# Kernel tuning notes

Hardware: AMD Instinct MI355X
Metric: run time of the kernel (lower is better)

## Reference

```python
import jax, jax.numpy as jnp
import numpy as np

N = 100000   # nodes
E = 1600000  # edges (before self loops)
H = 4        # heads
C = 32       # per-head channels
D = H * C    # hidden_dim = 128
G = 64       # graphs in batch
L = 4        # num_layers
IN_DIM = 7
NEG_SLOPE = 0.2


def setup_inputs() -> dict:
    key = jax.random.key(0)
    ks = jax.random.split(key, 14)
    s = 0.1
    x = jax.random.normal(ks[0], (N, IN_DIM), jnp.float32)
    edge_index = jax.random.randint(ks[1], (2, E), 0, N, dtype=jnp.int32)
    batch = jnp.sort(jax.random.randint(ks[2], (N,), 0, G, dtype=jnp.int32))
    W0 = jax.random.normal(ks[3], (IN_DIM, D), jnp.float32) * s
    a_src0 = jax.random.normal(ks[4], (H, C), jnp.float32) * s
    a_dst0 = jax.random.normal(ks[5], (H, C), jnp.float32) * s
    b0 = jnp.zeros((D,), jnp.float32)
    Ws = jax.random.normal(ks[6], (L - 1, D, D), jnp.float32) * s
    a_srcs = jax.random.normal(ks[7], (L - 1, H, C), jnp.float32) * s
    a_dsts = jax.random.normal(ks[8], (L - 1, H, C), jnp.float32) * s
    bs = jnp.zeros((L - 1, D), jnp.float32)
    ln_g = jnp.ones((L, D), jnp.float32)
    ln_b = jnp.zeros((L, D), jnp.float32)
    return dict(x=x, edge_index=edge_index, batch=batch, W0=W0, a_src0=a_src0,
                a_dst0=a_dst0, b0=b0, Ws=Ws, a_srcs=a_srcs, a_dsts=a_dsts,
                bs=bs, ln_g=ln_g, ln_b=ln_b)


def _gat_layer(x, W, a_src, a_dst, b, src, dst):
    # x: [N, F_in] -> h: [N, H, C] (PyG GATConv: shared lin for src/dst)
    h = (x @ W).reshape(N, H, C)
    alpha_src = jnp.einsum('nhc,hc->nh', h, a_src)  # [N, H]
    alpha_dst = jnp.einsum('nhc,hc->nh', h, a_dst)  # [N, H]
    logits = jax.nn.leaky_relu(alpha_src[src] + alpha_dst[dst], NEG_SLOPE)  # [E', H]
    # segment softmax over edges grouped by destination node
    m = jax.ops.segment_max(logits, dst, num_segments=N)          # [N, H]
    e = jnp.exp(logits - m[dst])
    z = jax.ops.segment_sum(e, dst, num_segments=N)               # [N, H]
    alpha = e / (z[dst] + 1e-16)                                  # [E', H]
    msg = h[src] * alpha[..., None]                               # [E', H, C]
    out = jax.ops.segment_sum(msg, dst, num_segments=N)           # [N, H, C]
    return out.reshape(N, D) + b


def _layernorm(x, g, b):
    mu = jnp.mean(x, axis=-1, keepdims=True)
    var = jnp.var(x, axis=-1, keepdims=True)
    return (x - mu) * jax.lax.rsqrt(var + 1e-5) * g + b


def reference(x, edge_index, batch, W0, a_src0, a_dst0, b0, Ws, a_srcs, a_dsts, bs, ln_g, ln_b):
    # PyG GATConv default: add self loops
    loop = jnp.arange(N, dtype=edge_index.dtype)
    src = jnp.concatenate([edge_index[0], loop])
    dst = jnp.concatenate([edge_index[1], loop])
    h = x
    for i in range(L):
        if i == 0:
            W, asr, ads, b = W0, a_src0, a_dst0, b0
        else:
            W, asr, ads, b = Ws[i - 1], a_srcs[i - 1], a_dsts[i - 1], bs[i - 1]
        h_new = _gat_layer(h, W, asr, ads, b, src, dst)
        h_new = jax.nn.elu(_layernorm(h_new, ln_g[i], ln_b[i]))
        h = h + h_new if i > 0 else h_new  # dropout is identity in eval
    node_embeddings = h  # [N, D]
    sums = jax.ops.segment_sum(node_embeddings, batch, num_segments=G)  # [G, D]
    cnt = jax.ops.segment_sum(jnp.ones((N,), node_embeddings.dtype), batch, num_segments=G)
    graph_embedding = sums / jnp.maximum(cnt, 1.0)[:, None]
    return node_embeddings, graph_embedding
```

## Files before the change

kernel.cpp:

```cpp
#include <hip/hip_runtime.h>
#include <hip/hip_bf16.h>

#define NN 100000
#define NE 1600000
#define NH 4
#define NC 32
#define DD 128
#define NG 64
#define NIN 7

#define BSH 9
#define NBUK ((NN + 511) >> BSH)
#define SEGCAP 9600
#define CAPE (SEGCAP - 512)
#define CSRN (NBUK * SEGCAP)
#define NBBIN ((NE + 4095)/4096)

typedef __hip_bfloat16 bf16;
typedef __attribute__((ext_vector_type(8))) short short8;
typedef __attribute__((ext_vector_type(4))) float f32x4;
typedef __attribute__((ext_vector_type(2))) float f32x2;

__device__ __forceinline__ float b2f(const bf16 v){ return __bfloat162float(v); }

__device__ __forceinline__ float in_ld(const void* p, size_t i, int f32){
  return f32 ? ((const float*)p)[i] : b2f(((const bf16*)p)[i]);
}

__device__ __forceinline__ unsigned int bfbits(float v){
  bf16 b = __float2bfloat16(v);
  return (unsigned int)(*(unsigned short*)&b);
}

__global__ __launch_bounds__(256) void k_init(float* __restrict__ gsum, int* __restrict__ gcnt,
                                              int* __restrict__ bcur,
                                              const unsigned int* __restrict__ xb, int* __restrict__ flag){
  int i = blockIdx.x*256 + threadIdx.x;
  if (i < NG*DD) gsum[i] = 0.f;
  if (i < NG) gcnt[i] = 0;
  if (i < NBUK) bcur[i] = i * CAPE;
  if (blockIdx.x == 0 && threadIdx.x < 64){
    int t = threadIdx.x;
    int pl = 0;
    for (int j = t; j < 512; j += 64){
      float v = __uint_as_float(xb[j]);
      float a = fabsf(v);
      if (v == v && a < 1e6f && a > 1e-10f) pl++;
    }
    #pragma unroll
    for (int off = 32; off > 0; off >>= 1) pl += __shfl_down(pl, off);
    if (t == 0) *flag = (pl >= 384) ? 1 : 0;
  }
}

__global__ __launch_bounds__(256) void k_bin(const int* __restrict__ src, const int* __restrict__ dst,
                                             int* __restrict__ bcur, int2* __restrict__ gstag,
                                             const void* __restrict__ Ws, bf16* __restrict__ WT,
                                             const int* __restrict__ flag){
  if (blockIdx.x >= NBBIN){
    int l = blockIdx.x - NBBIN;
    int f32 = *flag;
    for (int idx = threadIdx.x; idx < DD*DD; idx += 256){
      int n = idx >> 7, k = idx & 127;
      WT[(size_t)l*DD*DD + idx] = __float2bfloat16(in_ld(Ws, (size_t)l*DD*DD + (size_t)k*DD + n, f32));
    }
    return;
  }
  __shared__ int cnt[NBUK], pref[NBUK+1], place[NBUK], gbase[NBUK];
  __shared__ int2 pairs[4096];
  int tid = threadIdx.x;
  for (int b = tid; b < NBUK; b += 256){ cnt[b]=0; place[b]=0; }
  __syncthreads();
  int e0 = blockIdx.x*4096;
  int s[16], d[16];
  #pragma unroll
  for (int i=0;i<16;i++){
    int e = e0 + i*256 + tid;
    s[i] = 0; d[i] = -1;
    if (e < NE){
      unsigned int us = (unsigned int)src[e]; if (us >= NN) us = 0;
      unsigned int ud = (unsigned int)dst[e]; if (ud >= NN) ud = 0;
      s[i] = (int)us; d[i] = (int)ud;
      atomicAdd(&cnt[ud>>BSH], 1);
    }
  }
  __syncthreads();
  if (tid == 0){
    int run = 0;
    for (int b=0;b<NBUK;b++){ pref[b] = run; run += cnt[b]; }
    pref[NBUK] = run;
  }
  __syncthreads();
  for (int b = tid; b < NBUK; b += 256){
    if (cnt[b] > 0) gbase[b] = atomicAdd(&bcur[b], cnt[b]);
  }
  __syncthreads();
  #pragma unroll
  for (int i=0;i<16;i++){
    if (d[i] >= 0){
      int b = d[i]>>BSH;
      int lp = atomicAdd(&place[b],1);
      pairs[pref[b]+lp] = make_int2(s[i], d[i]);
    }
  }
  __syncthreads();
  int tot = pref[NBUK];
  for (int j = tid; j < tot; j += 256){
    int2 pr = pairs[j];
    int b = pr.y>>BSH;
    int gidx = gbase[b] + (j - pref[b]);
    if (gidx >= b*CAPE && gidx < (b+1)*CAPE) gstag[gidx] = pr;
  }
}

__global__ __launch_bounds__(256) void k_bucket(const int2* __restrict__ gstag,
                                                const int* __restrict__ bcur,
                                                int* __restrict__ csr,
                                                int* __restrict__ offs, int* __restrict__ oend){
  __shared__ int seg[SEGCAP];
  __shared__ int lcnt[512];
  __shared__ int loff[512];
  __shared__ int pscan[256];
  int b = blockIdx.x, tid = threadIdx.x;
  int nstart = b << BSH;
  int nend = min(nstart + 512, NN);
  int nloc = nend - nstart;
  int base = b * SEGCAP;
  int stbase = b * CAPE;
  int ecnt = bcur[b] - stbase;
  ecnt = max(0, min(ecnt, CAPE));
  lcnt[tid]     = (tid < nloc) ? 1 : 0;
  lcnt[tid+256] = (tid+256 < nloc) ? 1 : 0;
  __syncthreads();
  for (int j = tid; j < ecnt; j += 256){
    int2 pr = gstag[stbase + j];
    int ln = pr.y - nstart;
    if (ln < 0 || ln >= nloc) ln = 0;
    atomicAdd(&lcnt[ln], 1);
  }
  __syncthreads();
  int c0 = lcnt[2*tid], c1 = lcnt[2*tid+1];
  int pairsum = c0 + c1;
  pscan[tid] = pairsum;
  __syncthreads();
  for (int off=1; off<256; off<<=1){
    int a = (tid >= off) ? pscan[tid-off] : 0;
    __syncthreads();
    pscan[tid] += a;
    __syncthreads();
  }
  int pexcl = pscan[tid] - pairsum;
  loff[2*tid]   = pexcl;
  loff[2*tid+1] = pexcl + c0;
  __syncthreads();
  int segN = pscan[255];
  if (segN > SEGCAP) segN = SEGCAP;
  if (tid < nloc){
    offs[nstart + tid] = base + loff[tid];
    oend[nstart + tid] = base + loff[tid] + lcnt[tid];
  }
  if (tid + 256 < nloc){
    offs[nstart + tid + 256] = base + loff[tid+256];
    oend[nstart + tid + 256] = base + loff[tid+256] + lcnt[tid+256];
  }
  __syncthreads();
  if (tid < nloc){ int p = loff[tid]; if (p < SEGCAP) seg[p] = nstart + tid; lcnt[tid] = 1; }
  if (tid + 256 < nloc){ int p = loff[tid+256]; if (p < SEGCAP) seg[p] = nstart + tid + 256; lcnt[tid+256] = 1; }
  __syncthreads();
  for (int j = tid; j < ecnt; j += 256){
    int2 pr = gstag[stbase + j];
    int ln = pr.y - nstart;
    if (ln < 0 || ln >= nloc) ln = 0;
    int p = atomicAdd(&lcnt[ln], 1);
    int idx = loff[ln] + p;
    if (idx >= 0 && idx < SEGCAP) seg[idx] = pr.x;
  }
  __syncthreads();
  for (int j = tid; j < segN; j += 256) csr[base + j] = seg[j];
}

__device__ __forceinline__ void alpha_red(float acc, float was, float wad, int d, int n,
                                          float* __restrict__ asrc, float* __restrict__ adst){
  float ps = acc*was, pd = acc*wad;
  #pragma unroll
  for (int off=16; off>0; off>>=1){
    ps += __shfl_down(ps, off, 32);
    pd += __shfl_down(pd, off, 32);
  }
  if ((d & 31) == 0){
    asrc[n*NH + (d>>5)] = ps;
    adst[n*NH + (d>>5)] = pd;
  }
}

__global__ __launch_bounds__(128) void k_gemm0(const void* __restrict__ x, const void* __restrict__ W,
    const void* __restrict__ aws, const void* __restrict__ awd,
    bf16* __restrict__ hproj,
    float* __restrict__ asrc, float* __restrict__ adst, const int* __restrict__ flag){
  int f32 = *flag;
  __shared__ float xr[4][NIN];
  int d = threadIdx.x;
  int n0 = blockIdx.x*4;
  if (d < 4*NIN) xr[d/NIN][d%NIN] = in_ld(x, (size_t)n0*NIN + d, f32);
  __syncthreads();
  float a0=0,a1=0,a2=0,a3=0;
  #pragma unroll
  for (int k=0;k<NIN;k++){
    float w = in_ld(W, (size_t)k*DD + d, f32);
    a0 += xr[0][k]*w; a1 += xr[1][k]*w; a2 += xr[2][k]*w; a3 += xr[3][k]*w;
  }
  hproj[(size_t)(n0+0)*DD+d]=__float2bfloat16(a0);
  hproj[(size_t)(n0+1)*DD+d]=__float2bfloat16(a1);
  hproj[(size_t)(n0+2)*DD+d]=__float2bfloat16(a2);
  hproj[(size_t)(n0+3)*DD+d]=__float2bfloat16(a3);
  float was = in_ld(aws, d, f32), wad = in_ld(awd, d, f32);
  alpha_red(a0, was, wad, d, n0+0, asrc, adst);
  alpha_red(a1, was, wad, d, n0+1, asrc, adst);
  alpha_red(a2, was, wad, d, n0+2, asrc, adst);
  alpha_red(a3, was, wad, d, n0+3, asrc, adst);
}

#define LDA 136
#define LDB 136

__global__ __launch_bounds__(256) void k_gemm_mfma(
    const bf16* __restrict__ resid,
    const bf16* __restrict__ WT, size_t wtoff,
    const void* __restrict__ aws, const void* __restrict__ awd, size_t aoff,
    bf16* __restrict__ hproj,
    float* __restrict__ asrc, float* __restrict__ adst,
    const int* __restrict__ flag)
{
  __shared__ bf16 sA[64*LDA];
  __shared__ bf16 sB[128*LDB];
  int f32 = *flag;
  int t = threadIdx.x;
  int n0 = blockIdx.x*64;

  {
    const uint4* srcv = (const uint4*)(WT + wtoff);
    #pragma unroll
    for (int i=0;i<8;i++){
      int u4 = t + 256*i;
      int row = u4 >> 4, c = u4 & 15;
      *(uint4*)(&sB[row*LDB + c*8]) = srcv[u4];
    }
  }
  {
    const uint4* av = (const uint4*)resid;
    #pragma unroll
    for (int i=0;i<4;i++){
      int u4 = t + 256*i;
      int row = u4 >> 4, c = u4 & 15;
      int gr = n0 + row;
      uint4 v = make_uint4(0,0,0,0);
      if (gr < NN) v = av[(size_t)gr*16 + c];
      *(uint4*)(&sA[row*LDA + c*8]) = v;
    }
  }
  __syncthreads();

  int wv = t >> 6, lane = t & 63;
  int m = lane & 15, kq = lane >> 4;
  int rowbase = wv*16;

  f32x4 acc[8];
  #pragma unroll
  for (int nt=0; nt<8; nt++) acc[nt] = (f32x4){0.f,0.f,0.f,0.f};

  #pragma unroll
  for (int ks=0; ks<4; ks++){
    short8 afrag = *(const short8*)(&sA[(rowbase + m)*LDA + ks*32 + kq*8]);
    #pragma unroll
    for (int nt=0; nt<8; nt++){
      short8 bfrag = *(const short8*)(&sB[(nt*16 + m)*LDB + ks*32 + kq*8]);
      acc[nt] = __builtin_amdgcn_mfma_f32_16x16x32_bf16(afrag, bfrag, acc[nt], 0, 0, 0);
    }
  }

  #pragma unroll
  for (int reg=0; reg<4; reg++){
    int gr = n0 + rowbase + kq*4 + reg;
    if (gr < NN){
      bf16* dst = hproj + (size_t)gr*DD + m;
      #pragma unroll
      for (int nt=0; nt<8; nt++)
        dst[nt*16] = __float2bfloat16(acc[nt][reg]);
    }
  }

  float avs[8], avd[8];
  #pragma unroll
  for (int nt=0; nt<8; nt++){
    avs[nt] = in_ld(aws, aoff + nt*16 + m, f32);
    avd[nt] = in_ld(awd, aoff + nt*16 + m, f32);
  }
  #pragma unroll
  for (int h=0; h<4; h++){
    #pragma unroll
    for (int reg=0; reg<4; reg++){
      float ps = acc[2*h][reg]*avs[2*h] + acc[2*h+1][reg]*avs[2*h+1];
      float pd = acc[2*h][reg]*avd[2*h] + acc[2*h+1][reg]*avd[2*h+1];
      #pragma unroll
      for (int off=1; off<16; off<<=1){
        ps += __shfl_xor(ps, off);
        pd += __shfl_xor(pd, off);
      }
      if (m == 0){
        int gr = n0 + rowbase + kq*4 + reg;
        if (gr < NN){
          asrc[gr*NH + h] = ps;
          adst[gr*NH + h] = pd;
        }
      }
    }
  }
}

__device__ __forceinline__ float4 edge_e(const float4 as, const float4 ad){
  float4 l, e;
  l.x = as.x + ad.x; l.y = as.y + ad.y; l.z = as.z + ad.z; l.w = as.w + ad.w;
  l.x = l.x > 0.f ? l.x : 0.2f*l.x;
  l.y = l.y > 0.f ? l.y : 0.2f*l.y;
  l.z = l.z > 0.f ? l.z : 0.2f*l.z;
  l.w = l.w > 0.f ? l.w : 0.2f*l.w;
  l.x = fminf(l.x, 30.f); l.y = fminf(l.y, 30.f);
  l.z = fminf(l.z, 30.f); l.w = fminf(l.w, 30.f);
  e.x = __expf(l.x); e.y = __expf(l.y); e.z = __expf(l.z); e.w = __expf(l.w);
  return e;
}

__device__ __forceinline__ float2 hp_ld2(const void* hp, int s, int lane){
  unsigned int hv = ((const unsigned int*)hp)[(size_t)s*64 + lane];
  return make_float2(__uint_as_float(hv << 16), __uint_as_float(hv & 0xFFFF0000u));
}

__device__ __forceinline__ void fma_row(const uint4 hv, const float al,
                                        f32x2& a0, f32x2& a1, f32x2& a2, f32x2& a3){
  f32x2 v0 = {__uint_as_float(hv.x << 16), __uint_as_float(hv.x & 0xFFFF0000u)};
  f32x2 v1 = {__uint_as_float(hv.y << 16), __uint_as_float(hv.y & 0xFFFF0000u)};
  f32x2 v2 = {__uint_as_float(hv.z << 16), __uint_as_float(hv.z & 0xFFFF0000u)};
  f32x2 v3 = {__uint_as_float(hv.w << 16), __uint_as_float(hv.w & 0xFFFF0000u)};
  a0 += v0 * al;
  a1 += v1 * al;
  a2 += v2 * al;
  a3 += v3 * al;
}

template<int U>
__global__ __launch_bounds__(256) void k_agg(const bf16* __restrict__ hproj,
    const float* __restrict__ asrc, const float* __restrict__ adst,
    const int* __restrict__ offs, const int* __restrict__ oend, const int* __restrict__ csr,
    bf16* __restrict__ resid,
    const void* __restrict__ bias, size_t boff,
    const void* __restrict__ lng, const void* __restrict__ lnb, size_t lnoff,
    const int* __restrict__ flag, const int first)
{
  __shared__ float s_al[4][256];
  __shared__ int   s_off[4][64];
  int f32 = *flag;
  int wid = threadIdx.x >> 6, lane = threadIdx.x & 63;
  int n = blockIdx.x*4 + wid;
  int beg = offs[n];
  int end = oend[n];
  beg = max(0, min(beg, CSRN));
  end = max(beg, min(end, CSRN));
  int deg = min(end - beg, 1024);
  const float4 ad = ((const float4*)adst)[n];
  int head = lane >> 4;
  const char* hpB = (const char*)hproj;
  float2 acc;

  if (deg <= 64){
    float4 e = make_float4(0,0,0,0);
    if (lane < deg){
      unsigned int us = (unsigned int)csr[beg+lane];
      if (us >= NN) us = 0;
      s_off[wid][lane] = (int)(us << 8);
      float4 as = ((const float4*)asrc)[us];
      e = edge_e(as, ad);
    }
    float4 zs = e;
    #pragma unroll
    for (int off=32; off>0; off>>=1){
      zs.x += __shfl_down(zs.x, off);
      zs.y += __shfl_down(zs.y, off);
      zs.z += __shfl_down(zs.z, off);
      zs.w += __shfl_down(zs.w, off);
    }
    float4 invz;
    invz.x = 1.f/(__shfl(zs.x,0)+1e-16f);
    invz.y = 1.f/(__shfl(zs.y,0)+1e-16f);
    invz.z = 1.f/(__shfl(zs.z,0)+1e-16f);
    invz.w = 1.f/(__shfl(zs.w,0)+1e-16f);
    if (lane < deg){
      s_al[wid][lane*4+0] = e.x*invz.x;
      s_al[wid][lane*4+1] = e.y*invz.y;
      s_al[wid][lane*4+2] = e.z*invz.z;
      s_al[wid][lane*4+3] = e.w*invz.w;
    }
    __threadfence_block();

    int qg = lane >> 4;
    int ql = lane & 15;
    int hq = ql >> 2;
    int qbyte = ql << 4;
    f32x2 a0 = {0.f,0.f}, a1 = {0.f,0.f}, a2 = {0.f,0.f}, a3 = {0.f,0.f};
    int t = 0;
    for (; t+U <= deg; t += U){
      uint4 h[U/4];
      #pragma unroll
      for (int u=0; u<U/4; u++){
        int j = t + 4*u + qg;
        unsigned int off = (unsigned int)s_off[wid][j] + qbyte;
        h[u] = *(const uint4*)(hpB + off);
      }
      #pragma unroll
      for (int u=0; u<U/4; u++){
        int j = t + 4*u + qg;
        float al = s_al[wid][j*4 + hq];
        fma_row(h[u], al, a0, a1, a2, a3);
      }
    }
    for (; t+4 <= deg; t += 4){
      int j = t + qg;
      unsigned int off = (unsigned int)s_off[wid][j] + qbyte;
      const uint4 hv = *(const uint4*)(hpB + off);
      float al = s_al[wid][j*4 + hq];
      fma_row(hv, al, a0, a1, a2, a3);
    }
    if (t < deg){
      int j = t + qg;
      if (j < deg){
        unsigned int off = (unsigned int)s_off[wid][j] + qbyte;
        const uint4 hv = *(const uint4*)(hpB + off);
        float al = s_al[wid][j*4 + hq];
        fma_row(hv, al, a0, a1, a2, a3);
      }
    }

    #pragma unroll
    for (int off = 16; off < 64; off <<= 1){
      a0.x += __shfl_xor(a0.x, off); a0.y += __shfl_xor(a0.y, off);
      a1.x += __shfl_xor(a1.x, off); a1.y += __shfl_xor(a1.y, off);
      a2.x += __shfl_xor(a2.x, off); a2.y += __shfl_xor(a2.y, off);
      a3.x += __shfl_xor(a3.x, off); a3.y += __shfl_xor(a3.y, off);
    }
    __threadfence_block();
    if (qg == 0){
      float* red = &s_al[wid][0];
      red[ql*8+0] = a0.x; red[ql*8+1] = a0.y;
      red[ql*8+2] = a1.x; red[ql*8+3] = a1.y;
      red[ql*8+4] = a2.x; red[ql*8+5] = a2.y;
      red[ql*8+6] = a3.x; red[ql*8+7] = a3.y;
    }
    __threadfence_block();
    acc = make_float2(s_al[wid][2*lane], s_al[wid][2*lane+1]);
  } else {
    f32x2 ac0 = {0.f,0.f};
    float4 zs = make_float4(0,0,0,0);
    for (int j=lane; j<deg; j+=64){
      unsigned int us = (unsigned int)csr[beg+j];
      if (us >= NN) us = 0;
      float4 as = ((const float4*)asrc)[us];
      float4 e = edge_e(as, ad);
      zs.x+=e.x; zs.y+=e.y; zs.z+=e.z; zs.w+=e.w;
    }
    #pragma unroll
    for (int off=32; off>0; off>>=1){
      zs.x += __shfl_down(zs.x, off);
      zs.y += __shfl_down(zs.y, off);
      zs.z += __shfl_down(zs.z, off);
      zs.w += __shfl_down(zs.w, off);
    }
    float4 invz;
    invz.x = 1.f/(__shfl(zs.x,0)+1e-16f);
    invz.y = 1.f/(__shfl(zs.y,0)+1e-16f);
    invz.z = 1.f/(__shfl(zs.z,0)+1e-16f);
    invz.w = 1.f/(__shfl(zs.w,0)+1e-16f);
    int nch = (deg+63)>>6;
    for (int c2=0;c2<nch;c2++){
      int base = c2<<6, j = base+lane;
      int sreg = 0;
      __threadfence_block();
      if (j < deg){
        unsigned int us = (unsigned int)csr[beg+j];
        if (us >= NN) us = 0;
        sreg = (int)us;
        float4 as = ((const float4*)asrc)[us];
        float4 e = edge_e(as, ad);
        s_al[wid][lane*4+0]=e.x*invz.x;
        s_al[wid][lane*4+1]=e.y*invz.y;
        s_al[wid][lane*4+2]=e.z*invz.z;
        s_al[wid][lane*4+3]=e.w*invz.w;
      }
      __threadfence_block();
      int cnt = min(64, deg-base);
      for (int t2=0;t2<cnt;t2++){
        int s = __shfl(sreg, t2);
        float a = s_al[wid][t2*4+head];
        float2 hv = hp_ld2(hproj, s, lane);
        ac0.x += hv.x*a;
        ac0.y += hv.y*a;
      }
    }
    acc = make_float2(ac0.x, ac0.y);
  }

  float vx = acc.x + in_ld(bias, boff + 2*lane,   f32);
  float vy = acc.y + in_ld(bias, boff + 2*lane+1, f32);
  float s1 = vx+vy, s2 = vx*vx+vy*vy;
  #pragma unroll
  for (int off=32; off>0; off>>=1){
    s1 += __shfl_down(s1, off);
    s2 += __shfl_down(s2, off);
  }
  float mean = __shfl(s1,0) * (1.f/DD);
  float msq  = __shfl(s2,0) * (1.f/DD);
  float var  = fmaxf(msq - mean*mean, 0.f);
  float r = rsqrtf(var + 1e-5f);
  float yx = (vx-mean)*r*in_ld(lng, lnoff+2*lane,   f32) + in_ld(lnb, lnoff+2*lane,   f32);
  float yy = (vy-mean)*r*in_ld(lng, lnoff+2*lane+1, f32) + in_ld(lnb, lnoff+2*lane+1, f32);
  yx = yx>0.f ? yx : expm1f(yx);
  yy = yy>0.f ? yy : expm1f(yy);
  float2 res;
  if (first){
    res = make_float2(yx, yy);
  } else {
    unsigned int pu = ((const unsigned int*)resid)[(size_t)n*64 + lane];
    res = make_float2(__uint_as_float(pu << 16) + yx,
                      __uint_as_float(pu & 0xFFFF0000u) + yy);
  }
  unsigned int pk = bfbits(res.x) | (bfbits(res.y) << 16);
  ((unsigned int*)resid)[(size_t)n*64 + lane] = pk;
}

__global__ __launch_bounds__(256) void k_pool(const bf16* __restrict__ resid, void* __restrict__ dout,
    const int* __restrict__ batch, float* __restrict__ gsum, int* __restrict__ gcnt,
    const int* __restrict__ flag){
  __shared__ int sb[64];
  __shared__ float s_sum[2][DD];
  __shared__ int s_cnt[2];
  int f32 = *flag;
  int t = threadIdx.x;
  int s = t >> 4, ql = t & 15;
  int n0 = blockIdx.x*64;
  int cnt = min(64, NN - n0);
  if (t < 64){
    int bi = 0;
    if (t < cnt){
      unsigned int b = (unsigned int)batch[n0 + t];
      if (b >= NG) b = 0;
      bi = (int)b;
    }
    sb[t] = bi;
  }
  ((float*)s_sum)[t] = 0.f;
  if (t < 2) s_cnt[t] = 0;
  __syncthreads();
  int g0 = sb[0];
  int g1 = sb[cnt-1];
  if (t < cnt){
    int b = sb[t];
    if (b == g0) atomicAdd(&s_cnt[0], 1);
    else if (b == g1) atomicAdd(&s_cnt[1], 1);
    else atomicAdd(&gcnt[b], 1);
  }
  float acc0[8] = {0,0,0,0,0,0,0,0};
  float acc1[8] = {0,0,0,0,0,0,0,0};
  const uint4* rv = (const uint4*)resid;
  #pragma unroll
  for (int k=0;k<4;k++){
    int r = k*16 + s;
    if (r < cnt){
      int n = n0 + r;
      uint4 hv = rv[(size_t)n*16 + ql];
      float v[8];
      v[0]=__uint_as_float(hv.x<<16); v[1]=__uint_as_float(hv.x&0xFFFF0000u);
      v[2]=__uint_as_float(hv.y<<16); v[3]=__uint_as_float(hv.y&0xFFFF0000u);
      v[4]=__uint_as_float(hv.z<<16); v[5]=__uint_as_float(hv.z&0xFFFF0000u);
      v[6]=__uint_as_float(hv.w<<16); v[7]=__uint_as_float(hv.w&0xFFFF0000u);
      if (f32){
        float4* dp = (float4*)((char*)dout + (size_t)n*512 + ql*32);
        dp[0] = make_float4(v[0],v[1],v[2],v[3]);
        dp[1] = make_float4(v[4],v[5],v[6],v[7]);
      } else {
        *(uint4*)((char*)dout + (size_t)n*256 + ql*16) = hv;
      }
      int b = sb[r];
      if (b == g0){
        #pragma unroll
        for (int i=0;i<8;i++) acc0[i] += v[i];
      } else if (b == g1){
        #pragma unroll
        for (int i=0;i<8;i++) acc1[i] += v[i];
      } else {
        #pragma unroll
        for (int i=0;i<8;i++) atomicAdd(&gsum[b*DD + ql*8 + i], v[i]);
      }
    }
  }
  int c0 = ql*8;
  int twog = (g1 != g0);
  #pragma unroll
  for (int i=0;i<8;i++){
    atomicAdd(&s_sum[0][c0+i], acc0[i]);
    if (twog) atomicAdd(&s_sum[1][c0+i], acc1[i]);
  }
  __syncthreads();
  if (t < DD){
    atomicAdd(&gsum[g0*DD + t], s_sum[0][t]);
  } else if (twog && t < 2*DD){
    atomicAdd(&gsum[g1*DD + (t-DD)], s_sum[1][t-DD]);
  }
  if (t == 0){
    atomicAdd(&gcnt[g0], s_cnt[0]);
    if (twog) atomicAdd(&gcnt[g1], s_cnt[1]);
  }
}

__global__ __launch_bounds__(128) void k_final(const float* __restrict__ gsum, const int* __restrict__ gcnt,
                                               void* __restrict__ dout, const int* __restrict__ flag){
  int f32 = *flag;
  int i = blockIdx.x*128 + threadIdx.x;
  if (i < NG*DD){
    float c = (float)gcnt[i>>7];
    if (c < 1.f) c = 1.f;
    float val = gsum[i] / c;
    if (f32) ((float*)dout)[(size_t)NN*DD + i] = val;
    else     ((bf16*)dout)[(size_t)NN*DD + i] = __float2bfloat16(val);
  }
}

extern "C" void kernel_launch(void* const* d_in, const int* in_sizes, int n_in,
                              void* d_out, int out_size, void* d_ws, size_t ws_size,
                              hipStream_t stream){
  const void* x      = d_in[0];
  const int*  ei     = (const int*) d_in[1];
  const int*  batch  = (const int*) d_in[2];
  const void* W0     = d_in[3];
  const void* asrc0  = d_in[4];
  const void* adst0  = d_in[5];
  const void* b0     = d_in[6];
  const void* Ws     = d_in[7];
  const void* asrcs  = d_in[8];
  const void* adsts  = d_in[9];
  const void* bs     = d_in[10];
  const void* lng    = d_in[11];
  const void* lnb    = d_in[12];

  const int* srcs = ei;
  const int* dsts = ei + NE;

  uintptr_t p0 = (uintptr_t)d_ws;
  uintptr_t p = p0;
  auto alloc = [&](size_t bytes)->void* {
    void* r = (void*)p; p += (bytes + 255) & ~(size_t)255; return r;
  };
  int*   csr    = (int*)  alloc((size_t)CSRN*4);
  int*   offs   = (int*)  alloc((size_t)NN*4);
  int*   oend   = (int*)  alloc((size_t)NN*4);
  float* asrc   = (float*)alloc((size_t)NN*NH*4);
  float* adst   = (float*)alloc((size_t)NN*NH*4);
  float* gsum   = (float*)alloc((size_t)NG*DD*4);
  int*   gcnt   = (int*)  alloc(NG*4);
  int*   flag   = (int*)  alloc(256);
  int*   bcur   = (int*)  alloc((size_t)NBUK*4);
  int2*  gstag  = (int2*) alloc((size_t)NBUK*CAPE*8);
  bf16*  wt     = (bf16*) alloc((size_t)3*DD*DD*2);
  bf16*  hproj  = (bf16*) alloc((size_t)NN*DD*2);
  bf16*  resid  = (bf16*) alloc((size_t)NN*DD*2);

  const int NB = (NN + 255)/256;

  k_init<<<NB, 256, 0, stream>>>(gsum, gcnt, bcur, (const unsigned int*)x, flag);
  k_bin<<<NBBIN + 3, 256, 0, stream>>>(srcs, dsts, bcur, gstag, Ws, wt, flag);
  k_bucket<<<NBUK, 256, 0, stream>>>(gstag, bcur, csr, offs, oend);

  const int GEMM_B = (NN + 63)/64;

  k_gemm0<<<NN/4, 128, 0, stream>>>(x, W0, asrc0, adst0, hproj, asrc, adst, flag);
  k_agg<8><<<NN/4, 256, 0, stream>>>(hproj, asrc, adst, offs, oend, csr, resid,
                                     b0, 0, lng, lnb, 0, flag, 1);
  for (int l=1; l<4; l++){
    size_t wtoff = (size_t)(l-1)*DD*DD;
    size_t aoff  = (size_t)(l-1)*DD;
    k_gemm_mfma<<<GEMM_B, 256, 0, stream>>>(resid, wt, wtoff,
                                            asrcs, adsts, aoff,
                                            hproj, asrc, adst, flag);
    k_agg<8><<<NN/4, 256, 0, stream>>>(hproj, asrc, adst, offs, oend, csr, resid,
                                       bs, (size_t)(l-1)*DD, lng, lnb, (size_t)l*DD, flag, 0);
  }

  k_pool<<<(NN+63)/64, 256, 0, stream>>>(resid, d_out, batch, gsum, gcnt, flag);
  k_final<<<(NG*DD+127)/128, 128, 0, stream>>>(gsum, gcnt, d_out, flag);
}
```

Measured before the change: 615.1 us.

## Shrink CSR buckets to 256 nodes and double GEMM rows per block

Bucket sort now uses 256-node buckets with one node per thread, which simplifies the scan and doubles the number of bucket blocks so the CSR build has more parallelism. The MFMA projection GEMM now handles 128 rows per block, with each wave computing two 16-row tiles that share the same B fragments. This amortises the per-block weight load into LDS over twice as many rows, at the cost of more LDS and more accumulator registers. The smaller bucket capacity also gives less headroom for high-degree clusters before edges would overflow a bucket.

```diff
diff --git a/kernel.cpp b/kernel.cpp
--- a/kernel.cpp
+++ b/kernel.cpp
@@ -9,10 +9,10 @@
 #define NG 64
 #define NIN 7
 
-#define BSH 9
-#define NBUK ((NN + 511) >> BSH)
-#define SEGCAP 9600
-#define CAPE (SEGCAP - 512)
+#define BSH 8
+#define NBUK ((NN + 255) >> BSH)
+#define SEGCAP 4992
+#define CAPE (SEGCAP - 256)
 #define CSRN (NBUK * SEGCAP)
 #define NBBIN ((NE + 4095)/4096)
 
@@ -118,19 +118,18 @@
                                                 int* __restrict__ csr,
                                                 int* __restrict__ offs, int* __restrict__ oend){
   __shared__ int seg[SEGCAP];
-  __shared__ int lcnt[512];
-  __shared__ int loff[512];
-  __shared__ int pscan[256];
+  __shared__ int lcnt[256];
+  __shared__ int loff[256];
+  __shared__ int s_segN;
   int b = blockIdx.x, tid = threadIdx.x;
   int nstart = b << BSH;
-  int nend = min(nstart + 512, NN);
+  int nend = min(nstart + 256, NN);
   int nloc = nend - nstart;
   int base = b * SEGCAP;
   int stbase = b * CAPE;
   int ecnt = bcur[b] - stbase;
   ecnt = max(0, min(ecnt, CAPE));
-  lcnt[tid]     = (tid < nloc) ? 1 : 0;
-  lcnt[tid+256] = (tid+256 < nloc) ? 1 : 0;
+  lcnt[tid] = (tid < nloc) ? 1 : 0;
   __syncthreads();
   for (int j = tid; j < ecnt; j += 256){
     int2 pr = gstag[stbase + j];
@@ -139,33 +138,29 @@
     atomicAdd(&lcnt[ln], 1);
   }
   __syncthreads();
-  int c0 = lcnt[2*tid], c1 = lcnt[2*tid+1];
-  int pairsum = c0 + c1;
-  pscan[tid] = pairsum;
+  int own = lcnt[tid];
+  loff[tid] = own;
   __syncthreads();
   for (int off=1; off<256; off<<=1){
-    int a = (tid >= off) ? pscan[tid-off] : 0;
+    int a = (tid >= off) ? loff[tid-off] : 0;
     __syncthreads();
-    pscan[tid] += a;
+    loff[tid] += a;
     __syncthreads();
   }
-  int pexcl = pscan[tid] - pairsum;
-  loff[2*tid]   = pexcl;
-  loff[2*tid+1] = pexcl + c0;
-  __syncthreads();
-  int segN = pscan[255];
+  int incl = loff[tid];
+  if (tid == 255) s_segN = incl;
+  __syncthreads();
+  loff[tid] = incl - own;
+  __syncthreads();
+  int segN = s_segN;
   if (segN > SEGCAP) segN = SEGCAP;
   if (tid < nloc){
     offs[nstart + tid] = base + loff[tid];
-    oend[nstart + tid] = base + loff[tid] + lcnt[tid];
-  }
-  if (tid + 256 < nloc){
-    offs[nstart + tid + 256] = base + loff[tid+256];
-    oend[nstart + tid + 256] = base + loff[tid+256] + lcnt[tid+256];
-  }
-  __syncthreads();
-  if (tid < nloc){ int p = loff[tid]; if (p < SEGCAP) seg[p] = nstart + tid; lcnt[tid] = 1; }
-  if (tid + 256 < nloc){ int p = loff[tid+256]; if (p < SEGCAP) seg[p] = nstart + tid + 256; lcnt[tid+256] = 1; }
+    oend[nstart + tid] = base + loff[tid] + own;
+    int p = loff[tid];
+    if (p < SEGCAP) seg[p] = nstart + tid;
+    lcnt[tid] = 1;
+  }
   __syncthreads();
   for (int j = tid; j < ecnt; j += 256){
     int2 pr = gstag[stbase + j];
@@ -222,6 +217,7 @@
 
 #define LDA 136
 #define LDB 136
+#define GRPB 128
 
 __global__ __launch_bounds__(256) void k_gemm_mfma(
     const bf16* __restrict__ resid,
@@ -231,11 +227,11 @@
     float* __restrict__ asrc, float* __restrict__ adst,
     const int* __restrict__ flag)
 {
-  __shared__ bf16 sA[64*LDA];
+  __shared__ bf16 sA[GRPB*LDA];
   __shared__ bf16 sB[128*LDB];
   int f32 = *flag;
   int t = threadIdx.x;
-  int n0 = blockIdx.x*64;
+  int n0 = blockIdx.x*GRPB;
 
   {
     const uint4* srcv = (const uint4*)(WT + wtoff);
@@ -249,7 +245,7 @@
   {
     const uint4* av = (const uint4*)resid;
     #pragma unroll
-    for (int i=0;i<4;i++){
+    for (int i=0;i<8;i++){
       int u4 = t + 256*i;
       int row = u4 >> 4, c = u4 & 15;
       int gr = n0 + row;
@@ -262,30 +258,36 @@
 
   int wv = t >> 6, lane = t & 63;
   int m = lane & 15, kq = lane >> 4;
-  int rowbase = wv*16;
-
-  f32x4 acc[8];
-  #pragma unroll
-  for (int nt=0; nt<8; nt++) acc[nt] = (f32x4){0.f,0.f,0.f,0.f};
+
+  f32x4 acc[2][8];
+  #pragma unroll
+  for (int rg=0; rg<2; rg++)
+    #pragma unroll
+    for (int nt=0; nt<8; nt++) acc[rg][nt] = (f32x4){0.f,0.f,0.f,0.f};
 
   #pragma unroll
   for (int ks=0; ks<4; ks++){
-    short8 afrag = *(const short8*)(&sA[(rowbase + m)*LDA + ks*32 + kq*8]);
+    short8 af0 = *(const short8*)(&sA[(wv*32 +  0 + m)*LDA + ks*32 + kq*8]);
+    short8 af1 = *(const short8*)(&sA[(wv*32 + 16 + m)*LDA + ks*32 + kq*8]);
     #pragma unroll
     for (int nt=0; nt<8; nt++){
       short8 bfrag = *(const short8*)(&sB[(nt*16 + m)*LDB + ks*32 + kq*8]);
-      acc[nt] = __builtin_amdgcn_mfma_f32_16x16x32_bf16(afrag, bfrag, acc[nt], 0, 0, 0);
-    }
-  }
-
-  #pragma unroll
-  for (int reg=0; reg<4; reg++){
-    int gr = n0 + rowbase + kq*4 + reg;
-    if (gr < NN){
-      bf16* dst = hproj + (size_t)gr*DD + m;
-      #pragma unroll
-      for (int nt=0; nt<8; nt++)
-        dst[nt*16] = __float2bfloat16(acc[nt][reg]);
+      acc[0][nt] = __builtin_amdgcn_mfma_f32_16x16x32_bf16(af0, bfrag, acc[0][nt], 0, 0, 0);
+      acc[1][nt] = __builtin_amdgcn_mfma_f32_16x16x32_bf16(af1, bfrag, acc[1][nt], 0, 0, 0);
+    }
+  }
+
+  #pragma unroll
+  for (int rg=0; rg<2; rg++){
+    #pragma unroll
+    for (int reg=0; reg<4; reg++){
+      int gr = n0 + wv*32 + rg*16 + kq*4 + reg;
+      if (gr < NN){
+        bf16* dst = hproj + (size_t)gr*DD + m;
+        #pragma unroll
+        for (int nt=0; nt<8; nt++)
+          dst[nt*16] = __float2bfloat16(acc[rg][nt][reg]);
+      }
     }
   }
 
@@ -296,21 +298,24 @@
     avd[nt] = in_ld(awd, aoff + nt*16 + m, f32);
   }
   #pragma unroll
-  for (int h=0; h<4; h++){
-    #pragma unroll
-    for (int reg=0; reg<4; reg++){
-      float ps = acc[2*h][reg]*avs[2*h] + acc[2*h+1][reg]*avs[2*h+1];
-      float pd = acc[2*h][reg]*avd[2*h] + acc[2*h+1][reg]*avd[2*h+1];
+  for (int rg=0; rg<2; rg++){
+    #pragma unroll
+    for (int h=0; h<4; h++){
       #pragma unroll
-      for (int off=1; off<16; off<<=1){
-        ps += __shfl_xor(ps, off);
-        pd += __shfl_xor(pd, off);
-      }
-      if (m == 0){
-        int gr = n0 + rowbase + kq*4 + reg;
-        if (gr < NN){
-          asrc[gr*NH + h] = ps;
-          adst[gr*NH + h] = pd;
+      for (int reg=0; reg<4; reg++){
+        float ps = acc[rg][2*h][reg]*avs[2*h] + acc[rg][2*h+1][reg]*avs[2*h+1];
+        float pd = acc[rg][2*h][reg]*avd[2*h] + acc[rg][2*h+1][reg]*avd[2*h+1];
+        #pragma unroll
+        for (int off=1; off<16; off<<=1){
+          ps += __shfl_xor(ps, off);
+          pd += __shfl_xor(pd, off);
+        }
+        if (m == 0){
+          int gr = n0 + wv*32 + rg*16 + kq*4 + reg;
+          if (gr < NN){
+            asrc[gr*NH + h] = ps;
+            adst[gr*NH + h] = pd;
+          }
         }
       }
     }
@@ -677,7 +682,7 @@
   k_bin<<<NBBIN + 3, 256, 0, stream>>>(srcs, dsts, bcur, gstag, Ws, wt, flag);
   k_bucket<<<NBUK, 256, 0, stream>>>(gstag, bcur, csr, offs, oend);
 
-  const int GEMM_B = (NN + 63)/64;
+  const int GEMM_B = (NN + GRPB - 1)/GRPB;
 
   k_gemm0<<<NN/4, 128, 0, stream>>>(x, W0, asrc0, adst0, hproj, asrc, adst, flag);
   k_agg<8><<<NN/4, 256, 0, stream>>>(hproj, asrc, adst, offs, oend, csr, resid,
```

Result: no change. 621.8 us (+1.1%).
